# Kernel optimization log

Measured on AMD Instinct MI355X. Metric: run time of the kernel, lower is better.

Reference implementation:

```python
import jax, jax.numpy as jnp
import numpy as np

B, T, N, D = 8, 192, 64, 512
H = 8
DH = D // H
C = 8


def setup_inputs() -> dict:
    key = jax.random.key(0)
    ks = jax.random.split(key, 10)
    s = 1.0 / np.sqrt(D)
    return {
        "x": jax.random.normal(ks[0], (B, T, N, D), dtype=jnp.float32),
        "Wq_w": jax.random.normal(ks[1], (D, D), dtype=jnp.float32) * s,
        "Wq_b": jnp.zeros((D,), dtype=jnp.float32),
        "Wv_w": jax.random.normal(ks[2], (D, D), dtype=jnp.float32) * s,
        "Wv_b": jnp.zeros((D,), dtype=jnp.float32),
        "Wk": jax.random.normal(ks[3], (C, D, D), dtype=jnp.float32) * s,
        "bk": jnp.zeros((C, D), dtype=jnp.float32),
        "proj_w": jax.random.normal(ks[4], (D, D), dtype=jnp.float32) * s,
        "proj_b": jnp.zeros((D,), dtype=jnp.float32),
        "cluster_ids": jax.random.randint(ks[5], (N,), 0, C, dtype=jnp.int64),
    }


def reference(x, Wq_w, Wq_b, Wv_w, Wv_b, Wk, bk, proj_w, proj_b, cluster_ids):
    # torch Linear: y = x @ W.T + b
    Q = jnp.einsum('btnd,ed->btne', x, Wq_w) + Wq_b
    V = jnp.einsum('btnd,ed->btne', x, Wv_w) + Wv_b
    # per-cluster K projection == per-node weight gather (grouped GEMM)
    Wk_n = Wk[cluster_ids]          # [N, D, D]
    bk_n = bk[cluster_ids]          # [N, D]
    K = jnp.einsum('btnd,nde->btne', x, Wk_n) + bk_n

    def split_heads(z):
        # [B,T,N,D] -> [B,N,H,T,DH]
        return z.reshape(B, T, N, H, DH).transpose(0, 2, 3, 1, 4)

    Qh, Kh, Vh = split_heads(Q), split_heads(K), split_heads(V)
    scores = jnp.einsum('bnhtd,bnhsd->bnhts', Qh, Kh) / np.sqrt(DH).astype(np.float32)
    attn = jax.nn.softmax(scores, axis=-1)
    out_h = jnp.einsum('bnhts,bnhsd->bnhtd', attn, Vh)
    out = out_h.transpose(0, 3, 1, 2, 4).reshape(B, T, N, D)
    return jnp.einsum('btnd,ed->btne', out, proj_w) + proj_b
```

## Files before the change

### kernel.cpp

```cpp
#include <hip/hip_runtime.h>
#include <hip/hip_bf16.h>

typedef __bf16 bf16x8 __attribute__((ext_vector_type(8)));
typedef float  f32x4  __attribute__((ext_vector_type(4)));

#define MFMA16(a, b, c) __builtin_amdgcn_mfma_f32_16x16x32_bf16(a, b, c, 0, 0, 0)

__device__ __forceinline__ void async16(const __bf16* g, __bf16* l) {
    __builtin_amdgcn_global_load_lds(
        (const __attribute__((address_space(1))) unsigned int*)g,
        (__attribute__((address_space(3))) unsigned int*)l, 16, 0, 0);
}


__global__ void k_cast3(const float* __restrict__ wq, const float* __restrict__ wv,
                        const float* __restrict__ wp,
                        __bf16* __restrict__ oq, __bf16* __restrict__ ov,
                        __bf16* __restrict__ op) {
    int i = blockIdx.x * 256 + threadIdx.x;
    oq[i] = (__bf16)wq[i];
    ov[i] = (__bf16)wv[i];
    op[i] = (__bf16)wp[i];
}

__global__ void k_twk(const float* __restrict__ wk, __bf16* __restrict__ o) {
    int i = blockIdx.x * 256 + threadIdx.x;
    int c = i >> 18;
    int r = i & 262143;
    int d = r >> 9;
    int e = r & 511;
    o[(c << 18) + (e << 9) + d] = (__bf16)wk[i];
}

__global__ void k_castx(const float* __restrict__ x, __bf16* __restrict__ o) {
    size_t i = ((size_t)blockIdx.x * 256 + threadIdx.x) * 8;
    float4 f0 = *(const float4*)(x + i);
    float4 f1 = *(const float4*)(x + i + 4);
    bf16x8 v;
    v[0] = (__bf16)f0.x; v[1] = (__bf16)f0.y; v[2] = (__bf16)f0.z; v[3] = (__bf16)f0.w;
    v[4] = (__bf16)f1.x; v[5] = (__bf16)f1.y; v[6] = (__bf16)f1.z; v[7] = (__bf16)f1.w;
    *(bf16x8*)(o + i) = v;
}

__launch_bounds__(256)
__global__ void k_qkv(const __bf16* __restrict__ xb,
                      const __bf16* __restrict__ WqE, const __bf16* __restrict__ WvE,
                      const __bf16* __restrict__ WkE,
                      const float* __restrict__ bq, const float* __restrict__ bv,
                      const float* __restrict__ bk, const int* __restrict__ cid,
                      __bf16* __restrict__ Qw, __bf16* __restrict__ Kw,
                      __bf16* __restrict__ Vw) {
    const int n  = blockIdx.z;
    const int m0 = blockIdx.x * 128;
    const int e0 = blockIdx.y * 64;
    const int c  = cid[n];
    const __bf16* Wkc = WkE + ((size_t)c << 18);

    __shared__ __align__(16) __bf16 As[128 * 64];
    __shared__ __align__(16) __bf16 Bq[64 * 64];
    __shared__ __align__(16) __bf16 Bk[64 * 64];
    __shared__ __align__(16) __bf16 Bv[64 * 64];

    const int tid  = threadIdx.x;
    const int lane = tid & 63;
    const int w    = tid >> 6;
    const int wm   = w >> 1, wn = w & 1;
    const int l15  = lane & 15, qd = lane >> 4;
    const int lr   = lane >> 3;
    const int lc   = lane & 7;
    const int sc8  = (lc ^ lr) * 8;
    const int sw   = l15 & 7;

    const __bf16* ag = xb + ((size_t)(m0 + w * 32 + lr) * 64 + n) * 512 + sc8;
    __bf16*       al = As + w * 2048 + lr * 64 + lc * 8;
    const __bf16* qg = WqE + ((size_t)(e0 + w * 16 + lr) << 9) + sc8;
    const __bf16* kg = Wkc + ((size_t)(e0 + w * 16 + lr) << 9) + sc8;
    const __bf16* vg = WvE + ((size_t)(e0 + w * 16 + lr) << 9) + sc8;
    __bf16*       bl = Bq + w * 1024 + lr * 64 + lc * 8;
    __bf16*       kl = Bk + w * 1024 + lr * 64 + lc * 8;
    __bf16*       vl = Bv + w * 1024 + lr * 64 + lc * 8;

    f32x4 acc[3][4][2];
#pragma unroll
    for (int a = 0; a < 3; ++a)
#pragma unroll
        for (int i = 0; i < 4; ++i)
#pragma unroll
            for (int j = 0; j < 2; ++j) acc[a][i][j] = (f32x4){0.f, 0.f, 0.f, 0.f};

    for (int kk = 0; kk < 8; ++kk) {
        const int k0 = kk * 64;
        __syncthreads();
#pragma unroll
        for (int j = 0; j < 4; ++j) async16(ag + (size_t)j * 262144 + k0, al + j * 512);
#pragma unroll
        for (int j = 0; j < 2; ++j) {
            async16(qg + j * 4096 + k0, bl + j * 512);
            async16(kg + j * 4096 + k0, kl + j * 512);
            async16(vg + j * 4096 + k0, vl + j * 512);
        }
        __syncthreads();

#pragma unroll
        for (int kc = 0; kc < 2; ++kc) {
            const int co = ((kc * 4 + qd) ^ sw) * 8;
            bf16x8 a0 = *(const bf16x8*)&As[(wm * 64 + l15) * 64 + co];
            bf16x8 a1 = *(const bf16x8*)&As[(wm * 64 + 16 + l15) * 64 + co];
            bf16x8 a2 = *(const bf16x8*)&As[(wm * 64 + 32 + l15) * 64 + co];
            bf16x8 a3 = *(const bf16x8*)&As[(wm * 64 + 48 + l15) * 64 + co];
#pragma unroll
            for (int j = 0; j < 2; ++j) {
                const int bi = (wn * 32 + j * 16 + l15) * 64 + co;
                bf16x8 fq = *(const bf16x8*)&Bq[bi];
                bf16x8 fk = *(const bf16x8*)&Bk[bi];
                bf16x8 fv = *(const bf16x8*)&Bv[bi];
                acc[0][0][j] = MFMA16(a0, fq, acc[0][0][j]);
                acc[0][1][j] = MFMA16(a1, fq, acc[0][1][j]);
                acc[0][2][j] = MFMA16(a2, fq, acc[0][2][j]);
                acc[0][3][j] = MFMA16(a3, fq, acc[0][3][j]);
                acc[1][0][j] = MFMA16(a0, fk, acc[1][0][j]);
                acc[1][1][j] = MFMA16(a1, fk, acc[1][1][j]);
                acc[1][2][j] = MFMA16(a2, fk, acc[1][2][j]);
                acc[1][3][j] = MFMA16(a3, fk, acc[1][3][j]);
                acc[2][0][j] = MFMA16(a0, fv, acc[2][0][j]);
                acc[2][1][j] = MFMA16(a1, fv, acc[2][1][j]);
                acc[2][2][j] = MFMA16(a2, fv, acc[2][2][j]);
                acc[2][3][j] = MFMA16(a3, fv, acc[2][3][j]);
            }
        }
    }

    float biasq[2], biask[2], biasv[2];
#pragma unroll
    for (int j = 0; j < 2; ++j) {
        int e = e0 + wn * 32 + j * 16 + l15;
        biasq[j] = bq[e];
        biask[j] = bk[(c << 9) + e];
        biasv[j] = bv[e];
    }
#pragma unroll
    for (int i = 0; i < 4; ++i) {
#pragma unroll
        for (int rx = 0; rx < 4; ++rx) {
            int m  = m0 + wm * 64 + i * 16 + qd * 4 + rx;
            int bb = m / 192;
            int tt = m - bb * 192;
            size_t ro = ((size_t)(bb * 64 + n) * 192 + tt) << 9;
#pragma unroll
            for (int j = 0; j < 2; ++j) {
                int e = e0 + wn * 32 + j * 16 + l15;
                Qw[ro + e] = (__bf16)(acc[0][i][j][rx] + biasq[j]);
                Kw[ro + e] = (__bf16)(acc[1][i][j][rx] + biask[j]);
                Vw[ro + e] = (__bf16)(acc[2][i][j][rx] + biasv[j]);
            }
        }
    }
}

__launch_bounds__(768)
__global__ void k_attn(const __bf16* __restrict__ Qw, const __bf16* __restrict__ Kw,
                       const __bf16* __restrict__ Vw, __bf16* __restrict__ Ow) {
    const int h = blockIdx.x, n = blockIdx.y, b = blockIdx.z;
    __shared__ __align__(16) __bf16 Ks[192 * 72];
    __shared__ __align__(16) __bf16 Vt[64 * 192];
    __shared__ __align__(16) __bf16 Ps[192 * 200];

    const int tid  = threadIdx.x;
    const int lane = tid & 63, w = tid >> 6;
    const int l15  = lane & 15, qd = lane >> 4;
    const size_t base = ((size_t)((b * 64 + n) * 192) << 9) + h * 64;

    for (int i = tid; i < 1536; i += 768) {
        int row = i >> 3, pp = i & 7;
        *(bf16x8*)&Ks[row * 72 + 8 * pp] =
            *(const bf16x8*)(Kw + base + ((size_t)row << 9) + 8 * pp);
    }
#pragma unroll
    for (int rr = 0; rr < 2; ++rr) {
        int idx = rr * 768 + tid;
        int e = idx & 63, sb = idx >> 6;
        bf16x8 v;
#pragma unroll
        for (int j = 0; j < 8; ++j)
            v[j] = Vw[base + (size_t)(sb * 8 + j) * 512 + e];
        *(bf16x8*)&Vt[e * 192 + ((sb ^ (e & 7)) * 8)] = v;
    }
    __syncthreads();

    const __bf16* qp = Qw + base + ((size_t)(16 * w + l15) << 9) + 8 * qd;
    bf16x8 aq0 = *(const bf16x8*)(qp);
    bf16x8 aq1 = *(const bf16x8*)(qp + 32);

    f32x4 S[12];
#pragma unroll
    for (int ct = 0; ct < 12; ++ct) {
        f32x4 acc = (f32x4){0.f, 0.f, 0.f, 0.f};
        bf16x8 b0 = *(const bf16x8*)&Ks[(16 * ct + l15) * 72 + 8 * qd];
        bf16x8 b1 = *(const bf16x8*)&Ks[(16 * ct + l15) * 72 + 32 + 8 * qd];
        acc = MFMA16(aq0, b0, acc);
        acc = MFMA16(aq1, b1, acc);
        S[ct] = acc;
    }

    float mx[4] = {-1e30f, -1e30f, -1e30f, -1e30f};
#pragma unroll
    for (int ct = 0; ct < 12; ++ct)
#pragma unroll
        for (int rx = 0; rx < 4; ++rx) mx[rx] = fmaxf(mx[rx], S[ct][rx]);
#pragma unroll
    for (int mk = 1; mk < 16; mk <<= 1)
#pragma unroll
        for (int rx = 0; rx < 4; ++rx) mx[rx] = fmaxf(mx[rx], __shfl_xor(mx[rx], mk, 64));

    const float sc = 0.125f * 1.44269504088896f;
    float sm[4] = {0.f, 0.f, 0.f, 0.f};
#pragma unroll
    for (int ct = 0; ct < 12; ++ct) {
#pragma unroll
        for (int rx = 0; rx < 4; ++rx) {
            float pe = exp2f((S[ct][rx] - mx[rx]) * sc);
            sm[rx] += pe;
            Ps[(w * 16 + qd * 4 + rx) * 200 + 16 * ct + l15] = (__bf16)pe;
        }
    }
#pragma unroll
    for (int mk = 1; mk < 16; mk <<= 1)
#pragma unroll
        for (int rx = 0; rx < 4; ++rx) sm[rx] += __shfl_xor(sm[rx], mk, 64);

    __syncthreads();

    float inv[4];
#pragma unroll
    for (int rx = 0; rx < 4; ++rx) inv[rx] = 1.f / sm[rx];

#pragma unroll
    for (int et = 0; et < 4; ++et) {
        f32x4 acc = (f32x4){0.f, 0.f, 0.f, 0.f};
#pragma unroll
        for (int sn = 0; sn < 6; ++sn) {
            bf16x8 pa = *(const bf16x8*)&Ps[(w * 16 + l15) * 200 + sn * 32 + 8 * qd];
            bf16x8 vb = *(const bf16x8*)
                &Vt[(et * 16 + l15) * 192 + (((sn * 4 + qd) ^ (l15 & 7)) * 8)];
            acc = MFMA16(pa, vb, acc);
        }
#pragma unroll
        for (int rx = 0; rx < 4; ++rx) {
            int t = 16 * w + 4 * qd + rx;
            Ow[base + ((size_t)t << 9) + et * 16 + l15] = (__bf16)(acc[rx] * inv[rx]);
        }
    }
}

__launch_bounds__(256)
__global__ void k_proj(const __bf16* __restrict__ Ow, const __bf16* __restrict__ WpE,
                       const float* __restrict__ bp, float* __restrict__ out) {
    const int n  = blockIdx.z;
    const int m0 = blockIdx.x * 128;
    const int e0 = blockIdx.y * 128;
    __shared__ __align__(16) __bf16 As[128 * 64];
    __shared__ __align__(16) __bf16 Bs[128 * 64];

    const int tid  = threadIdx.x;
    const int lane = tid & 63, w = tid >> 6;
    const int wm   = w >> 1, wn = w & 1;
    const int l15  = lane & 15, qd = lane >> 4;
    const int lr   = lane >> 3, lc = lane & 7;
    const int sc8  = (lc ^ lr) * 8;
    const int sw   = l15 & 7;

    const __bf16* agj[4];
#pragma unroll
    for (int j = 0; j < 4; ++j) {
        int m  = m0 + w * 32 + j * 8 + lr;
        int bb = m / 192;
        int tt = m - bb * 192;
        agj[j] = Ow + (((size_t)(bb * 64 + n) * 192 + tt) << 9) + sc8;
    }
    __bf16* al = As + w * 2048 + lr * 64 + lc * 8;
    const __bf16* bg  = WpE + ((size_t)(e0 + w * 32 + lr) << 9) + sc8;
    __bf16*       blp = Bs + w * 2048 + lr * 64 + lc * 8;

    f32x4 acc[4][4];
#pragma unroll
    for (int i = 0; i < 4; ++i)
#pragma unroll
        for (int j = 0; j < 4; ++j) acc[i][j] = (f32x4){0.f, 0.f, 0.f, 0.f};

    for (int kk = 0; kk < 8; ++kk) {
        const int k0 = kk * 64;
        __syncthreads();
#pragma unroll
        for (int j = 0; j < 4; ++j) {
            async16(agj[j] + k0, al + j * 512);
            async16(bg + j * 4096 + k0, blp + j * 512);
        }
        __syncthreads();

#pragma unroll
        for (int kc = 0; kc < 2; ++kc) {
            const int co = ((kc * 4 + qd) ^ sw) * 8;
            bf16x8 a0 = *(const bf16x8*)&As[(wm * 64 + l15) * 64 + co];
            bf16x8 a1 = *(const bf16x8*)&As[(wm * 64 + 16 + l15) * 64 + co];
            bf16x8 a2 = *(const bf16x8*)&As[(wm * 64 + 32 + l15) * 64 + co];
            bf16x8 a3 = *(const bf16x8*)&As[(wm * 64 + 48 + l15) * 64 + co];
#pragma unroll
            for (int j = 0; j < 4; ++j) {
                bf16x8 fb = *(const bf16x8*)&Bs[(wn * 64 + j * 16 + l15) * 64 + co];
                acc[0][j] = MFMA16(a0, fb, acc[0][j]);
                acc[1][j] = MFMA16(a1, fb, acc[1][j]);
                acc[2][j] = MFMA16(a2, fb, acc[2][j]);
                acc[3][j] = MFMA16(a3, fb, acc[3][j]);
            }
        }
    }

    float bias[4];
#pragma unroll
    for (int j = 0; j < 4; ++j) bias[j] = bp[e0 + wn * 64 + j * 16 + l15];
#pragma unroll
    for (int i = 0; i < 4; ++i) {
#pragma unroll
        for (int rx = 0; rx < 4; ++rx) {
            int m = m0 + wm * 64 + i * 16 + qd * 4 + rx;
            size_t ro = ((size_t)(m * 64 + n)) << 9;
#pragma unroll
            for (int j = 0; j < 4; ++j) {
                int e = e0 + wn * 64 + j * 16 + l15;
                out[ro + e] = acc[i][j][rx] + bias[j];
            }
        }
    }
}

extern "C" void kernel_launch(void* const* d_in, const int* in_sizes, int n_in,
                              void* d_out, int out_size, void* d_ws, size_t ws_size,
                              hipStream_t stream) {
    const float* x    = (const float*)d_in[0];
    const float* Wq_w = (const float*)d_in[1];
    const float* Wq_b = (const float*)d_in[2];
    const float* Wv_w = (const float*)d_in[3];
    const float* Wv_b = (const float*)d_in[4];
    const float* Wk   = (const float*)d_in[5];
    const float* bk   = (const float*)d_in[6];
    const float* Wp   = (const float*)d_in[7];
    const float* bp   = (const float*)d_in[8];
    const int*   cid  = (const int*)d_in[9];
    float* out = (float*)d_out;

    __bf16* WqE = (__bf16*)d_ws;
    __bf16* WvE = WqE + (1 << 18);
    __bf16* WpE = WvE + (1 << 18);
    __bf16* WkE = WpE + (1 << 18);
    __bf16* Qw  = WkE + (8 << 18);
    __bf16* Kw  = Qw + 50331648LL;
    __bf16* Vw  = Kw + 50331648LL;
    __bf16* XO  = Vw + 50331648LL;

    k_cast3<<<1024, 256, 0, stream>>>(Wq_w, Wv_w, Wp, WqE, WvE, WpE);
    k_twk<<<8192, 256, 0, stream>>>(Wk, WkE);
    k_castx<<<24576, 256, 0, stream>>>(x, XO);
    k_qkv<<<dim3(12, 8, 64), 256, 0, stream>>>(XO, WqE, WvE, WkE, Wq_b, Wv_b, bk, cid,
                                               Qw, Kw, Vw);
    k_attn<<<dim3(8, 64, 8), 768, 0, stream>>>(Qw, Kw, Vw, XO);
    k_proj<<<dim3(12, 4, 64), 256, 0, stream>>>(XO, WpE, bp, out);
}
```

Measured before the change: 818.4 us.

## Restructure QKV GEMM into 256x256 double-buffered tiles with XCD-aware block remap

Rewrites the QKV projection kernel to use 512-thread blocks that each compute a 256x256 output tile of one projection (Q, V or K selected per block), instead of 128x64 tiles of all three projections. LDS is double-buffered so the next K slice loads asynchronously while MFMAs run, with explicit barriers, waitcnts and setprio around the MFMA bursts. The flat block index is permuted so consecutive blocks share a node across XCDs for better L2 reuse. This raises arithmetic intensity per loaded byte but uses 128 KB of LDS and 128 accumulator registers per thread, which may limit occupancy.

```diff
diff --git a/kernel.cpp b/kernel.cpp
--- a/kernel.cpp
+++ b/kernel.cpp
@@ -42,7 +42,7 @@
     *(bf16x8*)(o + i) = v;
 }
 
-__launch_bounds__(256)
+__launch_bounds__(512, 2)
 __global__ void k_qkv(const __bf16* __restrict__ xb,
                       const __bf16* __restrict__ WqE, const __bf16* __restrict__ WvE,
                       const __bf16* __restrict__ WkE,
@@ -50,108 +50,120 @@
                       const float* __restrict__ bk, const int* __restrict__ cid,
                       __bf16* __restrict__ Qw, __bf16* __restrict__ Kw,
                       __bf16* __restrict__ Vw) {
-    const int n  = blockIdx.z;
-    const int m0 = blockIdx.x * 128;
-    const int e0 = blockIdx.y * 64;
-    const int c  = cid[n];
-    const __bf16* Wkc = WkE + ((size_t)c << 18);
-
-    __shared__ __align__(16) __bf16 As[128 * 64];
-    __shared__ __align__(16) __bf16 Bq[64 * 64];
-    __shared__ __align__(16) __bf16 Bk[64 * 64];
-    __shared__ __align__(16) __bf16 Bv[64 * 64];
+    const int g   = blockIdx.y * 36 + blockIdx.x;
+    const int s   = (g & 7) * 288 + (g >> 3);
+    const int n   = s / 36;
+    const int r36 = s - n * 36;
+    const int mx  = r36 / 6;
+    const int ey  = r36 - mx * 6;
+    const int m0  = mx * 256;
+    const int e0  = ey * 256;
+    const int seg  = e0 >> 9;
+    const int eoff = e0 & 511;
+    const int c    = cid[n];
+
+    const __bf16* Wb = (seg == 0) ? WqE : (seg == 1) ? WvE : (WkE + ((size_t)c << 18));
+    __bf16*       Ob = (seg == 0) ? Qw : (seg == 1) ? Vw : Kw;
+
+    __shared__ __align__(16) __bf16 As[2][256 * 64];
+    __shared__ __align__(16) __bf16 Bs[2][256 * 64];
 
     const int tid  = threadIdx.x;
     const int lane = tid & 63;
     const int w    = tid >> 6;
-    const int wm   = w >> 1, wn = w & 1;
+    const int wm2  = w >> 2;
+    const int wn4  = w & 3;
     const int l15  = lane & 15, qd = lane >> 4;
-    const int lr   = lane >> 3;
-    const int lc   = lane & 7;
-    const int sc8  = (lc ^ lr) * 8;
-    const int sw   = l15 & 7;
-
-    const __bf16* ag = xb + ((size_t)(m0 + w * 32 + lr) * 64 + n) * 512 + sc8;
-    __bf16*       al = As + w * 2048 + lr * 64 + lc * 8;
-    const __bf16* qg = WqE + ((size_t)(e0 + w * 16 + lr) << 9) + sc8;
-    const __bf16* kg = Wkc + ((size_t)(e0 + w * 16 + lr) << 9) + sc8;
-    const __bf16* vg = WvE + ((size_t)(e0 + w * 16 + lr) << 9) + sc8;
-    __bf16*       bl = Bq + w * 1024 + lr * 64 + lc * 8;
-    __bf16*       kl = Bk + w * 1024 + lr * 64 + lc * 8;
-    __bf16*       vl = Bv + w * 1024 + lr * 64 + lc * 8;
-
-    f32x4 acc[3][4][2];
-#pragma unroll
-    for (int a = 0; a < 3; ++a)
-#pragma unroll
-        for (int i = 0; i < 4; ++i)
-#pragma unroll
-            for (int j = 0; j < 2; ++j) acc[a][i][j] = (f32x4){0.f, 0.f, 0.f, 0.f};
-
-    for (int kk = 0; kk < 8; ++kk) {
-        const int k0 = kk * 64;
-        __syncthreads();
-#pragma unroll
-        for (int j = 0; j < 4; ++j) async16(ag + (size_t)j * 262144 + k0, al + j * 512);
-#pragma unroll
-        for (int j = 0; j < 2; ++j) {
-            async16(qg + j * 4096 + k0, bl + j * 512);
-            async16(kg + j * 4096 + k0, kl + j * 512);
-            async16(vg + j * 4096 + k0, vl + j * 512);
-        }
-        __syncthreads();
-
-#pragma unroll
-        for (int kc = 0; kc < 2; ++kc) {
-            const int co = ((kc * 4 + qd) ^ sw) * 8;
-            bf16x8 a0 = *(const bf16x8*)&As[(wm * 64 + l15) * 64 + co];
-            bf16x8 a1 = *(const bf16x8*)&As[(wm * 64 + 16 + l15) * 64 + co];
-            bf16x8 a2 = *(const bf16x8*)&As[(wm * 64 + 32 + l15) * 64 + co];
-            bf16x8 a3 = *(const bf16x8*)&As[(wm * 64 + 48 + l15) * 64 + co];
-#pragma unroll
-            for (int j = 0; j < 2; ++j) {
-                const int bi = (wn * 32 + j * 16 + l15) * 64 + co;
-                bf16x8 fq = *(const bf16x8*)&Bq[bi];
-                bf16x8 fk = *(const bf16x8*)&Bk[bi];
-                bf16x8 fv = *(const bf16x8*)&Bv[bi];
-                acc[0][0][j] = MFMA16(a0, fq, acc[0][0][j]);
-                acc[0][1][j] = MFMA16(a1, fq, acc[0][1][j]);
-                acc[0][2][j] = MFMA16(a2, fq, acc[0][2][j]);
-                acc[0][3][j] = MFMA16(a3, fq, acc[0][3][j]);
-                acc[1][0][j] = MFMA16(a0, fk, acc[1][0][j]);
-                acc[1][1][j] = MFMA16(a1, fk, acc[1][1][j]);
-                acc[1][2][j] = MFMA16(a2, fk, acc[1][2][j]);
-                acc[1][3][j] = MFMA16(a3, fk, acc[1][3][j]);
-                acc[2][0][j] = MFMA16(a0, fv, acc[2][0][j]);
-                acc[2][1][j] = MFMA16(a1, fv, acc[2][1][j]);
-                acc[2][2][j] = MFMA16(a2, fv, acc[2][2][j]);
-                acc[2][3][j] = MFMA16(a3, fv, acc[2][3][j]);
-            }
-        }
-    }
-
-    float biasq[2], biask[2], biasv[2];
-#pragma unroll
-    for (int j = 0; j < 2; ++j) {
-        int e = e0 + wn * 32 + j * 16 + l15;
-        biasq[j] = bq[e];
-        biask[j] = bk[(c << 9) + e];
-        biasv[j] = bv[e];
-    }
-#pragma unroll
-    for (int i = 0; i < 4; ++i) {
+
+    const int sr  = tid >> 3;
+    const int sch = tid & 7;
+    const int sw8 = (sch ^ (sr & 7)) * 8;
+    const __bf16* aG = xb + ((size_t)(m0 + sr) * 64 + n) * 512 + sw8;
+    const __bf16* bG = Wb + ((size_t)(eoff + sr) << 9) + sw8;
+    const int ldst = tid * 8;
+
+    const int co0  = (qd ^ (l15 & 7)) * 8;
+    const int arow = wm2 * 128 + l15;
+    const int brow = wn4 * 64 + l15;
+
+    f32x4 acc[8][4];
+#pragma unroll
+    for (int i = 0; i < 8; ++i)
+#pragma unroll
+        for (int j = 0; j < 4; ++j) acc[i][j] = (f32x4){0.f, 0.f, 0.f, 0.f};
+
+#pragma unroll
+    for (int q = 0; q < 4; ++q) {
+        async16(aG + (size_t)q * 2097152, &As[0][q * 4096 + ldst]);
+        async16(bG + (size_t)q * 32768,   &Bs[0][q * 4096 + ldst]);
+    }
+    asm volatile("s_waitcnt vmcnt(0)" ::: "memory");
+    __builtin_amdgcn_s_barrier();
+
+    bf16x8 bfr[4][2];
+    for (int kt = 0; kt < 8; ++kt) {
+        const int cb = kt & 1, nb = cb ^ 1;
+        const int kn = (kt + 1) * 64;
+#pragma unroll
+        for (int q = 0; q < 4; ++q) {
+            if (q < 2 && kt < 7) {
+#pragma unroll
+                for (int h = 0; h < 2; ++h) {
+                    const int sl = 2 * q + h;
+                    async16(aG + (size_t)sl * 2097152 + kn, &As[nb][sl * 4096 + ldst]);
+                    async16(bG + (size_t)sl * 32768 + kn,   &Bs[nb][sl * 4096 + ldst]);
+                }
+            }
+            if (q == 0) {
+#pragma unroll
+                for (int j = 0; j < 4; ++j) {
+                    bfr[j][0] = *(const bf16x8*)&Bs[cb][(brow + j * 16) * 64 + co0];
+                    bfr[j][1] = *(const bf16x8*)&Bs[cb][(brow + j * 16) * 64 + (co0 ^ 32)];
+                }
+            }
+            bf16x8 a00 = *(const bf16x8*)&As[cb][(arow + (2 * q) * 16) * 64 + co0];
+            bf16x8 a01 = *(const bf16x8*)&As[cb][(arow + (2 * q) * 16) * 64 + (co0 ^ 32)];
+            bf16x8 a10 = *(const bf16x8*)&As[cb][(arow + (2 * q + 1) * 16) * 64 + co0];
+            bf16x8 a11 = *(const bf16x8*)&As[cb][(arow + (2 * q + 1) * 16) * 64 + (co0 ^ 32)];
+
+            __builtin_amdgcn_s_barrier();
+            asm volatile("s_waitcnt lgkmcnt(0)" ::: "memory");
+            __builtin_amdgcn_sched_barrier(0);
+            __builtin_amdgcn_s_setprio(1);
+#pragma unroll
+            for (int j = 0; j < 4; ++j) {
+                acc[2 * q][j]     = MFMA16(a00, bfr[j][0], acc[2 * q][j]);
+                acc[2 * q + 1][j] = MFMA16(a10, bfr[j][0], acc[2 * q + 1][j]);
+            }
+#pragma unroll
+            for (int j = 0; j < 4; ++j) {
+                acc[2 * q][j]     = MFMA16(a01, bfr[j][1], acc[2 * q][j]);
+                acc[2 * q + 1][j] = MFMA16(a11, bfr[j][1], acc[2 * q + 1][j]);
+            }
+            __builtin_amdgcn_s_setprio(0);
+            if (q == 3) asm volatile("s_waitcnt vmcnt(0)" ::: "memory");
+            __builtin_amdgcn_s_barrier();
+        }
+    }
+
+    float bias[4];
+#pragma unroll
+    for (int j = 0; j < 4; ++j) {
+        int e = eoff + wn4 * 64 + j * 16 + l15;
+        bias[j] = (seg == 0) ? bq[e] : (seg == 1) ? bv[e] : bk[(c << 9) + e];
+    }
+#pragma unroll
+    for (int i = 0; i < 8; ++i) {
 #pragma unroll
         for (int rx = 0; rx < 4; ++rx) {
-            int m  = m0 + wm * 64 + i * 16 + qd * 4 + rx;
+            int m  = m0 + wm2 * 128 + i * 16 + qd * 4 + rx;
             int bb = m / 192;
             int tt = m - bb * 192;
             size_t ro = ((size_t)(bb * 64 + n) * 192 + tt) << 9;
 #pragma unroll
-            for (int j = 0; j < 2; ++j) {
-                int e = e0 + wn * 32 + j * 16 + l15;
-                Qw[ro + e] = (__bf16)(acc[0][i][j][rx] + biasq[j]);
-                Kw[ro + e] = (__bf16)(acc[1][i][j][rx] + biask[j]);
-                Vw[ro + e] = (__bf16)(acc[2][i][j][rx] + biasv[j]);
+            for (int j = 0; j < 4; ++j) {
+                int e = eoff + wn4 * 64 + j * 16 + l15;
+                Ob[ro + e] = (__bf16)(acc[i][j][rx] + bias[j]);
             }
         }
     }
@@ -360,8 +372,8 @@
     k_cast3<<<1024, 256, 0, stream>>>(Wq_w, Wv_w, Wp, WqE, WvE, WpE);
     k_twk<<<8192, 256, 0, stream>>>(Wk, WkE);
     k_castx<<<24576, 256, 0, stream>>>(x, XO);
-    k_qkv<<<dim3(12, 8, 64), 256, 0, stream>>>(XO, WqE, WvE, WkE, Wq_b, Wv_b, bk, cid,
-                                               Qw, Kw, Vw);
+    k_qkv<<<dim3(36, 64), 512, 0, stream>>>(XO, WqE, WvE, WkE, Wq_b, Wv_b, bk, cid,
+                                            Qw, Kw, Vw);
     k_attn<<<dim3(8, 64, 8), 768, 0, stream>>>(Qw, Kw, Vw, XO);
     k_proj<<<dim3(12, 4, 64), 256, 0, stream>>>(XO, WpE, bp, out);
 }
```

Measured after the change: 862.0 us. +5.3%, slower.
